# Kernel optimization log

Hardware: AMD Instinct MI355X
Metric: run time of the kernel (lower is better)

The kernel has to match this reference:

```python
import jax, jax.numpy as jnp
import numpy as np

B, S, DM, H = 4, 2048, 768, 12
HD = DM // H
HEAD_Z = float(np.sqrt(HD))


def norm_layer(x, scale, bias):
    # custom normalization over last dim: (x - mean)/std * scale + bias, scalar scale/bias, no eps
    mean = x.mean(axis=2, keepdims=True)
    std = jnp.sqrt(((x - mean) ** 2).mean(axis=2, keepdims=True))
    return (x - mean) / std * scale + bias


def setup_inputs() -> dict:
    key = jax.random.key(0)
    ks = jax.random.split(key, 12)
    s = 1.0 / np.sqrt(DM)
    return {
        "base": jax.random.normal(ks[0], (B, S, DM), dtype=jnp.float32),
        "Wqkv": jax.random.normal(ks[1], (DM, 3 * DM), dtype=jnp.float32) * s,
        "bqkv": jax.random.normal(ks[2], (3 * DM,), dtype=jnp.float32) * s,
        "W1": jax.random.normal(ks[3], (DM, DM), dtype=jnp.float32) * s,
        "b1": jax.random.normal(ks[4], (DM,), dtype=jnp.float32) * s,
        "W2": jax.random.normal(ks[5], (DM, DM), dtype=jnp.float32) * s,
        "b2": jax.random.normal(ks[6], (DM,), dtype=jnp.float32) * s,
        "n1_scale": jax.random.uniform(ks[7], (1,), jnp.float32, -s, s) + 0.5,
        "n1_bias": jax.random.uniform(ks[8], (1,), jnp.float32, -s, s),
        "n2_scale": jax.random.uniform(ks[9], (1,), jnp.float32, -s, s) + 0.5,
        "n2_bias": jax.random.uniform(ks[10], (1,), jnp.float32, -s, s),
    }


def reference(base, Wqkv, bqkv, W1, b1, W2, b2, n1_scale, n1_bias, n2_scale, n2_bias):
    qkv = base @ Wqkv + bqkv                     # [B,S,3*DM]
    q, k, v = jnp.split(qkv, 3, axis=2)
    # per-head attention, vectorized over heads: the torch loop with broadcast-mul-sum
    # is mathematically softmax(QK^T/sqrt(hd)) @ V per head
    q = q.reshape(B, S, H, HD)
    k = k.reshape(B, S, H, HD)
    v = v.reshape(B, S, H, HD)
    scores = jnp.einsum('bqhd,bkhd->bhqk', q, k) / HEAD_Z  # [B,H,S,S]
    attn = jax.nn.softmax(scores, axis=-1)
    av = jnp.einsum('bhqk,bkhd->bqhd', attn, v).reshape(B, S, DM)
    hidden = norm_layer(av @ W1 + b1 + base, n1_scale, n1_bias)
    out = norm_layer(jax.nn.relu(hidden @ W2 + b2) + hidden, n2_scale, n2_bias)
    return out
```

## Files before the change

### kernel.cpp

```cpp
#include <hip/hip_runtime.h>
#include <hip/hip_bf16.h>
#include <stdint.h>

#define B_ 4
#define S_ 2048
#define DM_ 768
#define H_ 12
#define HD_ 64
#define ROWS (B_*S_)
#define QKVN (3*DM_)

typedef __attribute__((ext_vector_type(8))) short short8;
typedef __attribute__((ext_vector_type(4))) float floatx4;
typedef __attribute__((ext_vector_type(8))) unsigned short ushort8;
typedef __attribute__((ext_vector_type(4))) unsigned short ushort4v;
typedef __attribute__((ext_vector_type(4))) float float4_t;

__device__ __forceinline__ unsigned short f2b(float f) {
  union { float f; uint32_t u; } x; x.f = f;
  uint32_t r = x.u + 0x7FFFu + ((x.u >> 16) & 1u);
  return (unsigned short)(r >> 16);
}
__device__ __forceinline__ uint32_t fbits(float f) {
  union { float f; uint32_t u; } x; x.f = f; return x.u;
}

__device__ __forceinline__ void load_lds16(const void* g, void* l) {
  __builtin_amdgcn_global_load_lds(
      (const __attribute__((address_space(1))) uint32_t*)g,
      (__attribute__((address_space(3))) uint32_t*)l, 16, 0, 0);
}

__global__ __launch_bounds__(256) void cvt_bf16(const float* __restrict__ x,
                                                unsigned short* __restrict__ y, int n4) {
  int i = blockIdx.x * 256 + threadIdx.x;
  if (i < n4) {
    float4_t v = ((const float4_t*)x)[i];
    ushort4v o;
    o[0] = f2b(v[0]); o[1] = f2b(v[1]); o[2] = f2b(v[2]); o[3] = f2b(v[3]);
    ((ushort4v*)y)[i] = o;
  }
}

__global__ __launch_bounds__(256) void wtrans(const float* __restrict__ W,
                                              unsigned short* __restrict__ Wt,
                                              int K, int N) {
  __shared__ float t[32][33];
  int tx = threadIdx.x & 31, ty = threadIdx.x >> 5;
  int n0 = blockIdx.x * 32, k0 = blockIdx.y * 32;
#pragma unroll
  for (int i = 0; i < 4; i++)
    t[ty + i * 8][tx] = W[(size_t)(k0 + ty + i * 8) * N + n0 + tx];
  __syncthreads();
#pragma unroll
  for (int i = 0; i < 4; i++)
    Wt[(size_t)(n0 + ty + i * 8) * K + k0 + tx] = f2b(t[tx][ty + i * 8]);
}

__global__ __launch_bounds__(256) void vtrans(const unsigned short* __restrict__ qkv,
                                              unsigned short* __restrict__ Vt) {
  int st = blockIdx.x;
  int bh = blockIdx.y;
  int b = bh / H_, h = bh % H_;
  __shared__ unsigned short t[64][65];
  int tid = threadIdx.x;
#pragma unroll
  for (int i = 0; i < 2; i++) {
    int c = i * 256 + tid;
    int r = c >> 3, o = (c & 7) * 8;
    ushort8 v = *(const ushort8*)(qkv + (size_t)(b * S_ + st * 64 + r) * QKVN + 2 * DM_ + h * HD_ + o);
#pragma unroll
    for (int j = 0; j < 8; j++) t[r][o + j] = v[j];
  }
  __syncthreads();
#pragma unroll
  for (int i = 0; i < 2; i++) {
    int c = i * 256 + tid;
    int d = c >> 3, o = (c & 7) * 8;
    ushort8 v;
#pragma unroll
    for (int j = 0; j < 8; j++) {
      int p = o + j;
      int s = ((p & 3) << 4) | (p >> 2);
      v[j] = t[s][d];
    }
    *(ushort8*)(Vt + (size_t)(bh * 64 + d) * S_ + st * 64 + o) = v;
  }
}

template <int EPI>
__global__ __launch_bounds__(256, 3) void gemm_bf16(
    const unsigned short* __restrict__ A,
    const unsigned short* __restrict__ Bt,
    const float* __restrict__ bias,
    const float* __restrict__ res,
    void* __restrict__ Cout,
    int M, int N, int K) {
  __shared__ __align__(16) unsigned short As[128 * 64];
  __shared__ __align__(16) unsigned short Bs[128 * 64];
  int tid = threadIdx.x;
  int wave = tid >> 6, lane = tid & 63;
  int quad = lane >> 4, l16 = lane & 15;
  int e = l16 & 7;
  int sr = lane >> 3;
  int sc = (lane & 7) ^ (sr & 7);
  int m0 = blockIdx.y * 128, n0 = blockIdx.x * 128;
  int wm = (wave >> 1) * 64, wn = (wave & 1) * 64;
  floatx4 acc[4][4] = {};
  int c0 = wave * 4;

  for (int kb = 0; kb < K; kb += 64) {
#pragma unroll
    for (int i = 0; i < 4; i++) {
      int op = c0 + i;
      load_lds16(A + (size_t)(m0 + op * 8 + sr) * K + kb + sc * 8, (char*)As + op * 1024);
    }
#pragma unroll
    for (int i = 0; i < 4; i++) {
      int op = c0 + i;
      load_lds16(Bt + (size_t)(n0 + op * 8 + sr) * K + kb + sc * 8, (char*)Bs + op * 1024);
    }
    __syncthreads();
#pragma unroll
    for (int ks = 0; ks < 2; ks++) {
      short8 af[4], bfr[4];
#pragma unroll
      for (int mt = 0; mt < 4; mt++)
        af[mt] = *(const short8*)(As + (wm + mt * 16 + l16) * 64 + ((ks * 4 + quad) ^ e) * 8);
#pragma unroll
      for (int nt = 0; nt < 4; nt++)
        bfr[nt] = *(const short8*)(Bs + (wn + nt * 16 + l16) * 64 + ((ks * 4 + quad) ^ e) * 8);
#pragma unroll
      for (int mt = 0; mt < 4; mt++)
#pragma unroll
        for (int nt = 0; nt < 4; nt++)
          acc[mt][nt] = __builtin_amdgcn_mfma_f32_16x16x32_bf16(af[mt], bfr[nt], acc[mt][nt], 0, 0, 0);
    }
    __syncthreads();
  }
#pragma unroll
  for (int mt = 0; mt < 4; mt++) {
#pragma unroll
    for (int nt = 0; nt < 4; nt++) {
#pragma unroll
      for (int r = 0; r < 4; r++) {
        int row = m0 + wm + mt * 16 + quad * 4 + r;
        int col = n0 + wn + nt * 16 + l16;
        size_t idx = (size_t)row * N + col;
        float v = acc[mt][nt][r] + bias[col];
        if (EPI == 0) {
          ((unsigned short*)Cout)[idx] = f2b(v);
        } else if (EPI == 1) {
          ((float*)Cout)[idx] = v + res[idx];
        } else {
          ((float*)Cout)[idx] = fmaxf(v, 0.0f) + res[idx];
        }
      }
    }
  }
}

__global__ __launch_bounds__(256, 2) void attn(
    const unsigned short* __restrict__ qkv,
    const unsigned short* __restrict__ Vt,
    unsigned short* __restrict__ av) {
  int qt = blockIdx.x;
  int bh = blockIdx.y;
  int b = bh / H_, h = bh % H_;
  int row0 = b * S_ + qt * 128;
  __shared__ __align__(16) unsigned short Ks[2][64 * 64];
  __shared__ __align__(16) unsigned short Vs[2][64 * 64];
  __shared__ __align__(16) unsigned short Ps[4][32 * 72];
  int tid = threadIdx.x;
  int wave = tid >> 6, lane = tid & 63;
  int quad = lane >> 4, l16 = lane & 15;
  int e = l16 & 7;
  int sr = lane >> 3;
  int sc = (lane & 7) ^ (sr & 7);

#pragma unroll
  for (int i = 0; i < 4; i++) {
    load_lds16(qkv + (size_t)(row0 + wave * 32 + i * 8 + sr) * QKVN + h * HD_ + sc * 8,
               (char*)Ps[wave] + i * 1024);
  }
  auto stageKV = [&](int kt, int buf) {
#pragma unroll
    for (int i = 0; i < 2; i++) {
      int op = wave * 2 + i;
      load_lds16(qkv + (size_t)(b * S_ + kt * 64 + op * 8 + sr) * QKVN + DM_ + h * HD_ + sc * 8,
                 (char*)Ks[buf] + op * 1024);
      load_lds16(Vt + (size_t)(bh * 64 + op * 8 + sr) * S_ + kt * 64 + sc * 8,
                 (char*)Vs[buf] + op * 1024);
    }
  };
  stageKV(0, 0);

  floatx4 accO[2][4] = {};
  floatx4 accL[2] = {};
  const float scl = 0.125f * 1.44269504088896340736f;
  short8 ones;
#pragma unroll
  for (int j = 0; j < 8; j++) ones[j] = (short)0x3F80;
  __syncthreads();

  short8 qf[2][2];
#pragma unroll
  for (int mf = 0; mf < 2; mf++)
#pragma unroll
    for (int ks = 0; ks < 2; ks++)
      qf[mf][ks] = *(const short8*)(Ps[wave] + (mf * 16 + l16) * 64 + ((ks * 4 + quad) ^ e) * 8);

  int cur = 0;
  for (int kt = 0; kt < 32; kt++) {
    floatx4 sv[2][4] = {};
#pragma unroll
    for (int ks = 0; ks < 2; ks++)
#pragma unroll
      for (int nt = 0; nt < 4; nt++) {
        short8 kf = *(const short8*)(Ks[cur] + (nt * 16 + l16) * 64 + ((ks * 4 + quad) ^ e) * 8);
#pragma unroll
        for (int mf = 0; mf < 2; mf++)
          sv[mf][nt] = __builtin_amdgcn_mfma_f32_16x16x32_bf16(qf[mf][ks], kf, sv[mf][nt], 0, 0, 0);
      }
    if (kt + 1 < 32) stageKV(kt + 1, cur ^ 1);
#pragma unroll
    for (int mf = 0; mf < 2; mf++)
#pragma unroll
      for (int r = 0; r < 4; r++) {
        uint32_t u0 = fbits(__builtin_amdgcn_exp2f(sv[mf][0][r] * scl));
        uint32_t u1 = fbits(__builtin_amdgcn_exp2f(sv[mf][1][r] * scl));
        uint32_t u2 = fbits(__builtin_amdgcn_exp2f(sv[mf][2][r] * scl));
        uint32_t u3 = fbits(__builtin_amdgcn_exp2f(sv[mf][3][r] * scl));
        uint2 val;
        val.x = (u0 >> 16) | (u1 & 0xFFFF0000u);
        val.y = (u2 >> 16) | (u3 & 0xFFFF0000u);
        *(uint2*)(&Ps[wave][(mf * 16 + quad * 4 + r) * 72 + l16 * 4]) = val;
      }
#pragma unroll
    for (int ks = 0; ks < 2; ks++) {
      short8 pf[2];
#pragma unroll
      for (int mf = 0; mf < 2; mf++) {
        pf[mf] = *(const short8*)(Ps[wave] + (mf * 16 + l16) * 72 + ks * 32 + quad * 8);
        accL[mf] = __builtin_amdgcn_mfma_f32_16x16x32_bf16(pf[mf], ones, accL[mf], 0, 0, 0);
      }
#pragma unroll
      for (int nt = 0; nt < 4; nt++) {
        short8 vf = *(const short8*)(Vs[cur] + (nt * 16 + l16) * 64 + ((ks * 4 + quad) ^ e) * 8);
#pragma unroll
        for (int mf = 0; mf < 2; mf++)
          accO[mf][nt] = __builtin_amdgcn_mfma_f32_16x16x32_bf16(pf[mf], vf, accO[mf][nt], 0, 0, 0);
      }
    }
    __syncthreads();
    cur ^= 1;
  }
#pragma unroll
  for (int mf = 0; mf < 2; mf++)
#pragma unroll
    for (int r = 0; r < 4; r++) {
      float inv = 1.0f / accL[mf][r];
      int row = row0 + wave * 32 + mf * 16 + quad * 4 + r;
#pragma unroll
      for (int nt = 0; nt < 4; nt++)
        av[(size_t)row * DM_ + h * HD_ + nt * 16 + l16] = f2b(accO[mf][nt][r] * inv);
    }
}

template <int WB>
__global__ __launch_bounds__(256) void normk(
    const float* __restrict__ X, const float* __restrict__ scale,
    const float* __restrict__ bias, float* __restrict__ Y,
    unsigned short* __restrict__ Ybf) {
  int row = blockIdx.x;
  const float* x = X + (size_t)row * DM_;
  int tid = threadIdx.x;
  int wave = tid >> 6, lane = tid & 63;
  float v[3];
#pragma unroll
  for (int i = 0; i < 3; i++) v[i] = x[tid + i * 256];
  float s = v[0] + v[1] + v[2];
#pragma unroll
  for (int o = 32; o > 0; o >>= 1) s += __shfl_xor(s, o);
  __shared__ float red[4];
  if (lane == 0) red[wave] = s;
  __syncthreads();
  float mean = (red[0] + red[1] + red[2] + red[3]) * (1.0f / DM_);
  float ss = 0.0f;
#pragma unroll
  for (int i = 0; i < 3; i++) { v[i] -= mean; ss += v[i] * v[i]; }
#pragma unroll
  for (int o = 32; o > 0; o >>= 1) ss += __shfl_xor(ss, o);
  __syncthreads();
  if (lane == 0) red[wave] = ss;
  __syncthreads();
  float var = (red[0] + red[1] + red[2] + red[3]) * (1.0f / DM_);
  float rstd = rsqrtf(var);
  float sg = scale[0], bg = bias[0];
#pragma unroll
  for (int i = 0; i < 3; i++) {
    float y = v[i] * rstd * sg + bg;
    Y[(size_t)row * DM_ + tid + i * 256] = y;
    if (WB) Ybf[(size_t)row * DM_ + tid + i * 256] = f2b(y);
  }
}

extern "C" void kernel_launch(void* const* d_in, const int* in_sizes, int n_in,
                              void* d_out, int out_size, void* d_ws, size_t ws_size,
                              hipStream_t stream) {
  const float* base = (const float*)d_in[0];
  const float* Wqkv = (const float*)d_in[1];
  const float* bqkv = (const float*)d_in[2];
  const float* W1 = (const float*)d_in[3];
  const float* b1 = (const float*)d_in[4];
  const float* W2 = (const float*)d_in[5];
  const float* b2 = (const float*)d_in[6];
  const float* n1s = (const float*)d_in[7];
  const float* n1b = (const float*)d_in[8];
  const float* n2s = (const float*)d_in[9];
  const float* n2b = (const float*)d_in[10];
  float* out = (float*)d_out;

  char* ws = (char*)d_ws;
  size_t off = 0;
  auto alloc = [&](size_t bytes) {
    char* p = ws + off;
    off = (off + bytes + 255) & ~(size_t)255;
    return p;
  };
  unsigned short* base_bf = (unsigned short*)alloc((size_t)ROWS * DM_ * 2);
  unsigned short* Wqkvt = (unsigned short*)alloc((size_t)QKVN * DM_ * 2);
  unsigned short* W1t = (unsigned short*)alloc((size_t)DM_ * DM_ * 2);
  unsigned short* W2t = (unsigned short*)alloc((size_t)DM_ * DM_ * 2);
  unsigned short* qkvb = (unsigned short*)alloc((size_t)ROWS * QKVN * 2);
  unsigned short* Vtb = (unsigned short*)alloc((size_t)B_ * H_ * HD_ * S_ * 2);
  unsigned short* avb = (unsigned short*)alloc((size_t)ROWS * DM_ * 2);
  float* t1 = (float*)alloc((size_t)ROWS * DM_ * 4);
  float* hidden = (float*)alloc((size_t)ROWS * DM_ * 4);
  unsigned short* hbf = (unsigned short*)alloc((size_t)ROWS * DM_ * 2);

  cvt_bf16<<<ROWS * DM_ / 4 / 256, 256, 0, stream>>>(base, base_bf, ROWS * DM_ / 4);
  wtrans<<<dim3(QKVN / 32, DM_ / 32), 256, 0, stream>>>(Wqkv, Wqkvt, DM_, QKVN);
  wtrans<<<dim3(DM_ / 32, DM_ / 32), 256, 0, stream>>>(W1, W1t, DM_, DM_);
  wtrans<<<dim3(DM_ / 32, DM_ / 32), 256, 0, stream>>>(W2, W2t, DM_, DM_);
  gemm_bf16<0><<<dim3(QKVN / 128, ROWS / 128), 256, 0, stream>>>(
      base_bf, Wqkvt, bqkv, nullptr, qkvb, ROWS, QKVN, DM_);
  vtrans<<<dim3(S_ / 64, B_ * H_), 256, 0, stream>>>(qkvb, Vtb);
  attn<<<dim3(S_ / 128, B_ * H_), 256, 0, stream>>>(qkvb, Vtb, avb);
  gemm_bf16<1><<<dim3(DM_ / 128, ROWS / 128), 256, 0, stream>>>(
      avb, W1t, b1, base, t1, ROWS, DM_, DM_);
  normk<1><<<ROWS, 256, 0, stream>>>(t1, n1s, n1b, hidden, hbf);
  gemm_bf16<2><<<dim3(DM_ / 128, ROWS / 128), 256, 0, stream>>>(
      hbf, W2t, b2, hidden, t1, ROWS, DM_, DM_);
  normk<0><<<ROWS, 256, 0, stream>>>(t1, n2s, n2b, out, nullptr);
}
```

Baseline: 279.6 us.

## Merge prep kernels, add 64-row GEMM for DM-wide projections, use perm packing

Folds the bf16 conversion and the three weight transposes into one prep launch, which removes launch overhead. Adds a 64x128-tile GEMM used for the two 768-wide projections, doubling the block count (384 to 768) so the CUs are better filled on these small-N GEMMs. Replaces the shift/mask bf16 packing in attention with a single byte-permute instruction. Also lowers the main GEMM's occupancy hint from 3 to 2 blocks, which gives it more registers but may cut latency hiding.

```diff
diff --git a/kernel.cpp b/kernel.cpp
--- a/kernel.cpp
+++ b/kernel.cpp
@@ -31,23 +31,32 @@
       (__attribute__((address_space(3))) uint32_t*)l, 16, 0, 0);
 }
 
-__global__ __launch_bounds__(256) void cvt_bf16(const float* __restrict__ x,
-                                                unsigned short* __restrict__ y, int n4) {
-  int i = blockIdx.x * 256 + threadIdx.x;
-  if (i < n4) {
-    float4_t v = ((const float4_t*)x)[i];
+#define CVT_B 6144
+#define WQ_B 1728
+#define W1_B 576
+__global__ __launch_bounds__(256) void prep(
+    const float* __restrict__ base, unsigned short* __restrict__ base_bf,
+    const float* __restrict__ Wqkv, unsigned short* __restrict__ Wqkvt,
+    const float* __restrict__ W1, unsigned short* __restrict__ W1t,
+    const float* __restrict__ W2, unsigned short* __restrict__ W2t) {
+  __shared__ float t[32][33];
+  int bid = blockIdx.x;
+  int tid = threadIdx.x;
+  if (bid < CVT_B) {
+    int i = bid * 256 + tid;
+    float4_t v = ((const float4_t*)base)[i];
     ushort4v o;
     o[0] = f2b(v[0]); o[1] = f2b(v[1]); o[2] = f2b(v[2]); o[3] = f2b(v[3]);
-    ((ushort4v*)y)[i] = o;
-  }
-}
-
-__global__ __launch_bounds__(256) void wtrans(const float* __restrict__ W,
-                                              unsigned short* __restrict__ Wt,
-                                              int K, int N) {
-  __shared__ float t[32][33];
-  int tx = threadIdx.x & 31, ty = threadIdx.x >> 5;
-  int n0 = blockIdx.x * 32, k0 = blockIdx.y * 32;
+    ((ushort4v*)base_bf)[i] = o;
+    return;
+  }
+  const float* W; unsigned short* Wt; int N, rel;
+  if (bid < CVT_B + WQ_B)      { W = Wqkv; Wt = Wqkvt; N = QKVN; rel = bid - CVT_B; }
+  else if (bid < CVT_B + WQ_B + W1_B) { W = W1; Wt = W1t; N = DM_; rel = bid - CVT_B - WQ_B; }
+  else                          { W = W2; Wt = W2t; N = DM_; rel = bid - CVT_B - WQ_B - W1_B; }
+  int K = DM_;
+  int n0 = (rel % (N / 32)) * 32, k0 = (rel / (N / 32)) * 32;
+  int tx = tid & 31, ty = tid >> 5;
 #pragma unroll
   for (int i = 0; i < 4; i++)
     t[ty + i * 8][tx] = W[(size_t)(k0 + ty + i * 8) * N + n0 + tx];
@@ -89,7 +98,7 @@
 }
 
 template <int EPI>
-__global__ __launch_bounds__(256, 3) void gemm_bf16(
+__global__ __launch_bounds__(256, 2) void gemm_bf16(
     const unsigned short* __restrict__ A,
     const unsigned short* __restrict__ Bt,
     const float* __restrict__ bias,
@@ -160,6 +169,77 @@
   }
 }
 
+template <int EPI>
+__global__ __launch_bounds__(256, 4) void gemm64(
+    const unsigned short* __restrict__ A,
+    const unsigned short* __restrict__ Bt,
+    const float* __restrict__ bias,
+    const float* __restrict__ res,
+    void* __restrict__ Cout,
+    int M, int N, int K) {
+  __shared__ __align__(16) unsigned short As[64 * 64];
+  __shared__ __align__(16) unsigned short Bs[128 * 64];
+  int tid = threadIdx.x;
+  int wave = tid >> 6, lane = tid & 63;
+  int quad = lane >> 4, l16 = lane & 15;
+  int e = l16 & 7;
+  int sr = lane >> 3;
+  int sc = (lane & 7) ^ (sr & 7);
+  int m0 = blockIdx.y * 64, n0 = blockIdx.x * 128;
+  int wm = (wave >> 1) * 32, wn = (wave & 1) * 64;
+  floatx4 acc[2][4] = {};
+
+  for (int kb = 0; kb < K; kb += 64) {
+#pragma unroll
+    for (int i = 0; i < 2; i++) {
+      int op = wave * 2 + i;
+      load_lds16(A + (size_t)(m0 + op * 8 + sr) * K + kb + sc * 8, (char*)As + op * 1024);
+    }
+#pragma unroll
+    for (int i = 0; i < 4; i++) {
+      int op = wave * 4 + i;
+      load_lds16(Bt + (size_t)(n0 + op * 8 + sr) * K + kb + sc * 8, (char*)Bs + op * 1024);
+    }
+    __syncthreads();
+#pragma unroll
+    for (int ks = 0; ks < 2; ks++) {
+      short8 af[2], bfr[4];
+#pragma unroll
+      for (int mt = 0; mt < 2; mt++)
+        af[mt] = *(const short8*)(As + (wm + mt * 16 + l16) * 64 + ((ks * 4 + quad) ^ e) * 8);
+#pragma unroll
+      for (int nt = 0; nt < 4; nt++)
+        bfr[nt] = *(const short8*)(Bs + (wn + nt * 16 + l16) * 64 + ((ks * 4 + quad) ^ e) * 8);
+#pragma unroll
+      for (int mt = 0; mt < 2; mt++)
+#pragma unroll
+        for (int nt = 0; nt < 4; nt++)
+          acc[mt][nt] = __builtin_amdgcn_mfma_f32_16x16x32_bf16(af[mt], bfr[nt], acc[mt][nt], 0, 0, 0);
+    }
+    __syncthreads();
+  }
+#pragma unroll
+  for (int mt = 0; mt < 2; mt++) {
+#pragma unroll
+    for (int nt = 0; nt < 4; nt++) {
+#pragma unroll
+      for (int r = 0; r < 4; r++) {
+        int row = m0 + wm + mt * 16 + quad * 4 + r;
+        int col = n0 + wn + nt * 16 + l16;
+        size_t idx = (size_t)row * N + col;
+        float v = acc[mt][nt][r] + bias[col];
+        if (EPI == 0) {
+          ((unsigned short*)Cout)[idx] = f2b(v);
+        } else if (EPI == 1) {
+          ((float*)Cout)[idx] = v + res[idx];
+        } else {
+          ((float*)Cout)[idx] = fmaxf(v, 0.0f) + res[idx];
+        }
+      }
+    }
+  }
+}
+
 __global__ __launch_bounds__(256, 2) void attn(
     const unsigned short* __restrict__ qkv,
     const unsigned short* __restrict__ Vt,
@@ -232,8 +312,8 @@
         uint32_t u2 = fbits(__builtin_amdgcn_exp2f(sv[mf][2][r] * scl));
         uint32_t u3 = fbits(__builtin_amdgcn_exp2f(sv[mf][3][r] * scl));
         uint2 val;
-        val.x = (u0 >> 16) | (u1 & 0xFFFF0000u);
-        val.y = (u2 >> 16) | (u3 & 0xFFFF0000u);
+        val.x = __builtin_amdgcn_perm(u1, u0, 0x07060302u);
+        val.y = __builtin_amdgcn_perm(u3, u2, 0x07060302u);
         *(uint2*)(&Ps[wave][(mf * 16 + quad * 4 + r) * 72 + l16 * 4]) = val;
       }
 #pragma unroll
@@ -339,18 +419,16 @@
   float* hidden = (float*)alloc((size_t)ROWS * DM_ * 4);
   unsigned short* hbf = (unsigned short*)alloc((size_t)ROWS * DM_ * 2);
 
-  cvt_bf16<<<ROWS * DM_ / 4 / 256, 256, 0, stream>>>(base, base_bf, ROWS * DM_ / 4);
-  wtrans<<<dim3(QKVN / 32, DM_ / 32), 256, 0, stream>>>(Wqkv, Wqkvt, DM_, QKVN);
-  wtrans<<<dim3(DM_ / 32, DM_ / 32), 256, 0, stream>>>(W1, W1t, DM_, DM_);
-  wtrans<<<dim3(DM_ / 32, DM_ / 32), 256, 0, stream>>>(W2, W2t, DM_, DM_);
+  prep<<<CVT_B + WQ_B + 2 * W1_B, 256, 0, stream>>>(
+      base, base_bf, Wqkv, Wqkvt, W1, W1t, W2, W2t);
   gemm_bf16<0><<<dim3(QKVN / 128, ROWS / 128), 256, 0, stream>>>(
       base_bf, Wqkvt, bqkv, nullptr, qkvb, ROWS, QKVN, DM_);
   vtrans<<<dim3(S_ / 64, B_ * H_), 256, 0, stream>>>(qkvb, Vtb);
   attn<<<dim3(S_ / 128, B_ * H_), 256, 0, stream>>>(qkvb, Vtb, avb);
-  gemm_bf16<1><<<dim3(DM_ / 128, ROWS / 128), 256, 0, stream>>>(
+  gemm64<1><<<dim3(DM_ / 128, ROWS / 64), 256, 0, stream>>>(
       avb, W1t, b1, base, t1, ROWS, DM_, DM_);
   normk<1><<<ROWS, 256, 0, stream>>>(t1, n1s, n1b, hidden, hbf);
-  gemm_bf16<2><<<dim3(DM_ / 128, ROWS / 128), 256, 0, stream>>>(
+  gemm64<2><<<dim3(DM_ / 128, ROWS / 64), 256, 0, stream>>>(
       hbf, W2t, b2, hidden, t1, ROWS, DM_, DM_);
   normk<0><<<ROWS, 256, 0, stream>>>(t1, n2s, n2b, out, nullptr);
 }
```

Result: faster. 264.5 us (-5.4%).

## Fuse prep kernels, shrink GEMM M-tile to 64, widen attention waves to 64 rows

Applied to the files above, without the earlier changes.

Merges the bf16 conversion and three weight-transpose launches into one prep kernel to cut launch overhead. The GEMMs now use 64x128 tiles with higher occupancy, which doubles block count for better CU fill on the small N=768 GEMMs. Attention now uses 2 waves of 64 query rows each instead of 4 waves of 32, so each K/V fragment feeds more MFMAs, at the cost of more registers and fewer waves. The bf16 packing also switches to v_perm.

```diff
diff --git a/kernel.cpp b/kernel.cpp
--- a/kernel.cpp
+++ b/kernel.cpp
@@ -31,23 +31,32 @@
       (__attribute__((address_space(3))) uint32_t*)l, 16, 0, 0);
 }
 
-__global__ __launch_bounds__(256) void cvt_bf16(const float* __restrict__ x,
-                                                unsigned short* __restrict__ y, int n4) {
-  int i = blockIdx.x * 256 + threadIdx.x;
-  if (i < n4) {
-    float4_t v = ((const float4_t*)x)[i];
+#define CVT_B 6144
+#define WQ_B 1728
+#define W1_B 576
+__global__ __launch_bounds__(256) void prep(
+    const float* __restrict__ base, unsigned short* __restrict__ base_bf,
+    const float* __restrict__ Wqkv, unsigned short* __restrict__ Wqkvt,
+    const float* __restrict__ W1, unsigned short* __restrict__ W1t,
+    const float* __restrict__ W2, unsigned short* __restrict__ W2t) {
+  __shared__ float t[32][33];
+  int bid = blockIdx.x;
+  int tid = threadIdx.x;
+  if (bid < CVT_B) {
+    int i = bid * 256 + tid;
+    float4_t v = ((const float4_t*)base)[i];
     ushort4v o;
     o[0] = f2b(v[0]); o[1] = f2b(v[1]); o[2] = f2b(v[2]); o[3] = f2b(v[3]);
-    ((ushort4v*)y)[i] = o;
-  }
-}
-
-__global__ __launch_bounds__(256) void wtrans(const float* __restrict__ W,
-                                              unsigned short* __restrict__ Wt,
-                                              int K, int N) {
-  __shared__ float t[32][33];
-  int tx = threadIdx.x & 31, ty = threadIdx.x >> 5;
-  int n0 = blockIdx.x * 32, k0 = blockIdx.y * 32;
+    ((ushort4v*)base_bf)[i] = o;
+    return;
+  }
+  const float* W; unsigned short* Wt; int N, rel;
+  if (bid < CVT_B + WQ_B)      { W = Wqkv; Wt = Wqkvt; N = QKVN; rel = bid - CVT_B; }
+  else if (bid < CVT_B + WQ_B + W1_B) { W = W1; Wt = W1t; N = DM_; rel = bid - CVT_B - WQ_B; }
+  else                          { W = W2; Wt = W2t; N = DM_; rel = bid - CVT_B - WQ_B - W1_B; }
+  int K = DM_;
+  int n0 = (rel % (N / 32)) * 32, k0 = (rel / (N / 32)) * 32;
+  int tx = tid & 31, ty = tid >> 5;
 #pragma unroll
   for (int i = 0; i < 4; i++)
     t[ty + i * 8][tx] = W[(size_t)(k0 + ty + i * 8) * N + n0 + tx];
@@ -89,14 +98,14 @@
 }
 
 template <int EPI>
-__global__ __launch_bounds__(256, 3) void gemm_bf16(
+__global__ __launch_bounds__(256, 4) void gemm64(
     const unsigned short* __restrict__ A,
     const unsigned short* __restrict__ Bt,
     const float* __restrict__ bias,
     const float* __restrict__ res,
     void* __restrict__ Cout,
     int M, int N, int K) {
-  __shared__ __align__(16) unsigned short As[128 * 64];
+  __shared__ __align__(16) unsigned short As[64 * 64];
   __shared__ __align__(16) unsigned short Bs[128 * 64];
   int tid = threadIdx.x;
   int wave = tid >> 6, lane = tid & 63;
@@ -104,34 +113,33 @@
   int e = l16 & 7;
   int sr = lane >> 3;
   int sc = (lane & 7) ^ (sr & 7);
-  int m0 = blockIdx.y * 128, n0 = blockIdx.x * 128;
-  int wm = (wave >> 1) * 64, wn = (wave & 1) * 64;
-  floatx4 acc[4][4] = {};
-  int c0 = wave * 4;
+  int m0 = blockIdx.y * 64, n0 = blockIdx.x * 128;
+  int wm = (wave >> 1) * 32, wn = (wave & 1) * 64;
+  floatx4 acc[2][4] = {};
 
   for (int kb = 0; kb < K; kb += 64) {
 #pragma unroll
+    for (int i = 0; i < 2; i++) {
+      int op = wave * 2 + i;
+      load_lds16(A + (size_t)(m0 + op * 8 + sr) * K + kb + sc * 8, (char*)As + op * 1024);
+    }
+#pragma unroll
     for (int i = 0; i < 4; i++) {
-      int op = c0 + i;
-      load_lds16(A + (size_t)(m0 + op * 8 + sr) * K + kb + sc * 8, (char*)As + op * 1024);
-    }
-#pragma unroll
-    for (int i = 0; i < 4; i++) {
-      int op = c0 + i;
+      int op = wave * 4 + i;
       load_lds16(Bt + (size_t)(n0 + op * 8 + sr) * K + kb + sc * 8, (char*)Bs + op * 1024);
     }
     __syncthreads();
 #pragma unroll
     for (int ks = 0; ks < 2; ks++) {
-      short8 af[4], bfr[4];
-#pragma unroll
-      for (int mt = 0; mt < 4; mt++)
+      short8 af[2], bfr[4];
+#pragma unroll
+      for (int mt = 0; mt < 2; mt++)
         af[mt] = *(const short8*)(As + (wm + mt * 16 + l16) * 64 + ((ks * 4 + quad) ^ e) * 8);
 #pragma unroll
       for (int nt = 0; nt < 4; nt++)
         bfr[nt] = *(const short8*)(Bs + (wn + nt * 16 + l16) * 64 + ((ks * 4 + quad) ^ e) * 8);
 #pragma unroll
-      for (int mt = 0; mt < 4; mt++)
+      for (int mt = 0; mt < 2; mt++)
 #pragma unroll
         for (int nt = 0; nt < 4; nt++)
           acc[mt][nt] = __builtin_amdgcn_mfma_f32_16x16x32_bf16(af[mt], bfr[nt], acc[mt][nt], 0, 0, 0);
@@ -139,7 +147,7 @@
     __syncthreads();
   }
 #pragma unroll
-  for (int mt = 0; mt < 4; mt++) {
+  for (int mt = 0; mt < 2; mt++) {
 #pragma unroll
     for (int nt = 0; nt < 4; nt++) {
 #pragma unroll
@@ -160,7 +168,7 @@
   }
 }
 
-__global__ __launch_bounds__(256, 2) void attn(
+__global__ __launch_bounds__(128, 2) void attn(
     const unsigned short* __restrict__ qkv,
     const unsigned short* __restrict__ Vt,
     unsigned short* __restrict__ av) {
@@ -170,7 +178,7 @@
   int row0 = b * S_ + qt * 128;
   __shared__ __align__(16) unsigned short Ks[2][64 * 64];
   __shared__ __align__(16) unsigned short Vs[2][64 * 64];
-  __shared__ __align__(16) unsigned short Ps[4][32 * 72];
+  __shared__ __align__(16) unsigned short Ps[2][64 * 72];
   int tid = threadIdx.x;
   int wave = tid >> 6, lane = tid & 63;
   int quad = lane >> 4, l16 = lane & 15;
@@ -179,14 +187,14 @@
   int sc = (lane & 7) ^ (sr & 7);
 
 #pragma unroll
-  for (int i = 0; i < 4; i++) {
-    load_lds16(qkv + (size_t)(row0 + wave * 32 + i * 8 + sr) * QKVN + h * HD_ + sc * 8,
+  for (int i = 0; i < 8; i++) {
+    load_lds16(qkv + (size_t)(row0 + wave * 64 + i * 8 + sr) * QKVN + h * HD_ + sc * 8,
                (char*)Ps[wave] + i * 1024);
   }
   auto stageKV = [&](int kt, int buf) {
 #pragma unroll
-    for (int i = 0; i < 2; i++) {
-      int op = wave * 2 + i;
+    for (int i = 0; i < 4; i++) {
+      int op = wave * 4 + i;
       load_lds16(qkv + (size_t)(b * S_ + kt * 64 + op * 8 + sr) * QKVN + DM_ + h * HD_ + sc * 8,
                  (char*)Ks[buf] + op * 1024);
       load_lds16(Vt + (size_t)(bh * 64 + op * 8 + sr) * S_ + kt * 64 + sc * 8,
@@ -195,36 +203,36 @@
   };
   stageKV(0, 0);
 
-  floatx4 accO[2][4] = {};
-  floatx4 accL[2] = {};
+  floatx4 accO[4][4] = {};
+  floatx4 accL[4] = {};
   const float scl = 0.125f * 1.44269504088896340736f;
   short8 ones;
 #pragma unroll
   for (int j = 0; j < 8; j++) ones[j] = (short)0x3F80;
   __syncthreads();
 
-  short8 qf[2][2];
-#pragma unroll
-  for (int mf = 0; mf < 2; mf++)
+  short8 qf[4][2];
+#pragma unroll
+  for (int mf = 0; mf < 4; mf++)
 #pragma unroll
     for (int ks = 0; ks < 2; ks++)
       qf[mf][ks] = *(const short8*)(Ps[wave] + (mf * 16 + l16) * 64 + ((ks * 4 + quad) ^ e) * 8);
 
   int cur = 0;
   for (int kt = 0; kt < 32; kt++) {
-    floatx4 sv[2][4] = {};
+    floatx4 sv[4][4] = {};
 #pragma unroll
     for (int ks = 0; ks < 2; ks++)
 #pragma unroll
       for (int nt = 0; nt < 4; nt++) {
         short8 kf = *(const short8*)(Ks[cur] + (nt * 16 + l16) * 64 + ((ks * 4 + quad) ^ e) * 8);
 #pragma unroll
-        for (int mf = 0; mf < 2; mf++)
+        for (int mf = 0; mf < 4; mf++)
           sv[mf][nt] = __builtin_amdgcn_mfma_f32_16x16x32_bf16(qf[mf][ks], kf, sv[mf][nt], 0, 0, 0);
       }
     if (kt + 1 < 32) stageKV(kt + 1, cur ^ 1);
 #pragma unroll
-    for (int mf = 0; mf < 2; mf++)
+    for (int mf = 0; mf < 4; mf++)
 #pragma unroll
       for (int r = 0; r < 4; r++) {
         uint32_t u0 = fbits(__builtin_amdgcn_exp2f(sv[mf][0][r] * scl));
@@ -232,15 +240,15 @@
         uint32_t u2 = fbits(__builtin_amdgcn_exp2f(sv[mf][2][r] * scl));
         uint32_t u3 = fbits(__builtin_amdgcn_exp2f(sv[mf][3][r] * scl));
         uint2 val;
-        val.x = (u0 >> 16) | (u1 & 0xFFFF0000u);
-        val.y = (u2 >> 16) | (u3 & 0xFFFF0000u);
+        val.x = __builtin_amdgcn_perm(u1, u0, 0x07060302u);
+        val.y = __builtin_amdgcn_perm(u3, u2, 0x07060302u);
         *(uint2*)(&Ps[wave][(mf * 16 + quad * 4 + r) * 72 + l16 * 4]) = val;
       }
 #pragma unroll
     for (int ks = 0; ks < 2; ks++) {
-      short8 pf[2];
-#pragma unroll
-      for (int mf = 0; mf < 2; mf++) {
+      short8 pf[4];
+#pragma unroll
+      for (int mf = 0; mf < 4; mf++) {
         pf[mf] = *(const short8*)(Ps[wave] + (mf * 16 + l16) * 72 + ks * 32 + quad * 8);
         accL[mf] = __builtin_amdgcn_mfma_f32_16x16x32_bf16(pf[mf], ones, accL[mf], 0, 0, 0);
       }
@@ -248,7 +256,7 @@
       for (int nt = 0; nt < 4; nt++) {
         short8 vf = *(const short8*)(Vs[cur] + (nt * 16 + l16) * 64 + ((ks * 4 + quad) ^ e) * 8);
 #pragma unroll
-        for (int mf = 0; mf < 2; mf++)
+        for (int mf = 0; mf < 4; mf++)
           accO[mf][nt] = __builtin_amdgcn_mfma_f32_16x16x32_bf16(pf[mf], vf, accO[mf][nt], 0, 0, 0);
       }
     }
@@ -256,11 +264,11 @@
     cur ^= 1;
   }
 #pragma unroll
-  for (int mf = 0; mf < 2; mf++)
+  for (int mf = 0; mf < 4; mf++)
 #pragma unroll
     for (int r = 0; r < 4; r++) {
       float inv = 1.0f / accL[mf][r];
-      int row = row0 + wave * 32 + mf * 16 + quad * 4 + r;
+      int row = row0 + wave * 64 + mf * 16 + quad * 4 + r;
 #pragma unroll
       for (int nt = 0; nt < 4; nt++)
         av[(size_t)row * DM_ + h * HD_ + nt * 16 + l16] = f2b(accO[mf][nt][r] * inv);
@@ -339,18 +347,16 @@
   float* hidden = (float*)alloc((size_t)ROWS * DM_ * 4);
   unsigned short* hbf = (unsigned short*)alloc((size_t)ROWS * DM_ * 2);
 
-  cvt_bf16<<<ROWS * DM_ / 4 / 256, 256, 0, stream>>>(base, base_bf, ROWS * DM_ / 4);
-  wtrans<<<dim3(QKVN / 32, DM_ / 32), 256, 0, stream>>>(Wqkv, Wqkvt, DM_, QKVN);
-  wtrans<<<dim3(DM_ / 32, DM_ / 32), 256, 0, stream>>>(W1, W1t, DM_, DM_);
-  wtrans<<<dim3(DM_ / 32, DM_ / 32), 256, 0, stream>>>(W2, W2t, DM_, DM_);
-  gemm_bf16<0><<<dim3(QKVN / 128, ROWS / 128), 256, 0, stream>>>(
+  prep<<<CVT_B + WQ_B + 2 * W1_B, 256, 0, stream>>>(
+      base, base_bf, Wqkv, Wqkvt, W1, W1t, W2, W2t);
+  gemm64<0><<<dim3(QKVN / 128, ROWS / 64), 256, 0, stream>>>(
       base_bf, Wqkvt, bqkv, nullptr, qkvb, ROWS, QKVN, DM_);
   vtrans<<<dim3(S_ / 64, B_ * H_), 256, 0, stream>>>(qkvb, Vtb);
-  attn<<<dim3(S_ / 128, B_ * H_), 256, 0, stream>>>(qkvb, Vtb, avb);
-  gemm_bf16<1><<<dim3(DM_ / 128, ROWS / 128), 256, 0, stream>>>(
+  attn<<<dim3(S_ / 128, B_ * H_), 128, 0, stream>>>(qkvb, Vtb, avb);
+  gemm64<1><<<dim3(DM_ / 128, ROWS / 64), 256, 0, stream>>>(
       avb, W1t, b1, base, t1, ROWS, DM_, DM_);
   normk<1><<<ROWS, 256, 0, stream>>>(t1, n1s, n1b, hidden, hbf);
-  gemm_bf16<2><<<dim3(DM_ / 128, ROWS / 128), 256, 0, stream>>>(
+  gemm64<2><<<dim3(DM_ / 128, ROWS / 64), 256, 0, stream>>>(
       hbf, W2t, b2, hidden, t1, ROWS, DM_, DM_);
   normk<0><<<ROWS, 256, 0, stream>>>(t1, n2s, n2b, out, nullptr);
 }
```

Result: no change. 281.6 us (+0.7%).
